# Kernel tuning notes

Hardware: AMD Instinct MI355X
Metric: run time of the kernel (lower is better)

Reference implementation:

```python
import jax, jax.numpy as jnp
import numpy as np

# Block sizes: 3-hop sampled bipartite graphs (src -> dst per layer)
N_SRC0, N_DST0, E0 = 500_000, 100_000, 1_000_000
N_DST1, E1 = 10_000, 100_000
N_DST2, E2 = 1_024, 10_240
D_IN, D_HID, N_CLS = 128, 128, 47


def setup_inputs() -> dict:
    key = jax.random.key(0)
    ks = jax.random.split(key, 16)
    feats = jax.random.normal(ks[0], (N_SRC0, D_IN), dtype=jnp.float32)
    src0 = jax.random.randint(ks[1], (E0,), 0, N_SRC0)
    dst0 = jax.random.randint(ks[2], (E0,), 0, N_DST0)
    src1 = jax.random.randint(ks[3], (E1,), 0, N_DST0)
    dst1 = jax.random.randint(ks[4], (E1,), 0, N_DST1)
    src2 = jax.random.randint(ks[5], (E2,), 0, N_DST1)
    dst2 = jax.random.randint(ks[6], (E2,), 0, N_DST2)
    # fsi.inverse_idx reindex + NPFeatureShuffle all-to-all -> two permutations
    inverse_idx = jax.random.permutation(ks[7], N_DST0)
    shuffle_idx = jax.random.permutation(ks[8], N_DST0)
    def glorot(k, fan_in, fan_out):
        lim = np.sqrt(6.0 / (fan_in + fan_out)).astype(np.float32)
        return jax.random.uniform(k, (fan_in, fan_out), jnp.float32, -lim, lim)
    W0 = glorot(ks[9], D_IN, D_HID)
    b0 = jnp.zeros((D_HID,), jnp.float32)
    W1 = glorot(ks[10], D_HID, D_HID)
    b1 = jnp.zeros((D_HID,), jnp.float32)
    W2 = glorot(ks[11], D_HID, N_CLS)
    b2 = jnp.zeros((N_CLS,), jnp.float32)
    return dict(feats=feats, src0=src0, dst0=dst0, src1=src1, dst1=dst1,
                src2=src2, dst2=dst2, inverse_idx=inverse_idx,
                shuffle_idx=shuffle_idx, W0=W0, b0=b0, W1=W1, b1=b1, W2=W2, b2=b2)


def _graph_conv(h_src, src, dst, n_src, n_dst, W, b, norm_both):
    # DGL GraphConv: optional D^{-1/2} on src, W, sum-aggregate over edges,
    # optional D^{-1/2} on dst, + bias. Degrees clamped to min 1.
    ones = jnp.ones(src.shape[0], dtype=h_src.dtype)
    if norm_both:
        out_deg = jax.ops.segment_sum(ones, src, num_segments=n_src)
        h_src = h_src * jax.lax.rsqrt(jnp.clip(out_deg, 1.0, None))[:, None]
    msgs = (h_src @ W)[src]                      # [E, d_out] gather
    agg = jax.ops.segment_sum(msgs, dst, num_segments=n_dst)  # scatter-add
    if norm_both:
        in_deg = jax.ops.segment_sum(ones, dst, num_segments=n_dst)
        agg = agg * jax.lax.rsqrt(jnp.clip(in_deg, 1.0, None))[:, None]
    return agg + b


def reference(feats, src0, dst0, src1, dst1, src2, dst2,
              inverse_idx, shuffle_idx, W0, b0, W1, b1, W2, b2):
    # layer 0: norm='none'
    h = _graph_conv(feats, src0, dst0, N_SRC0, N_DST0, W0, b0, norm_both=False)
    # fsi.inverse_idx reindex + NPFeatureShuffle (modeled as permutations)
    h = h[inverse_idx]
    h = h[shuffle_idx]
    h = jax.nn.relu(h)  # dropout is identity in eval
    # layer 1: norm='both'
    h = _graph_conv(h, src1, dst1, N_DST0, N_DST1, W1, b1, norm_both=True)
    h = jax.nn.relu(h)
    # layer 2: norm='both'
    h = _graph_conv(h, src2, dst2, N_DST1, N_DST2, W2, b2, norm_both=True)
    return h
```

## Files before the change

### kernel.cpp

```cpp
#include <hip/hip_runtime.h>
#include <stdint.h>

typedef unsigned int u32;
typedef unsigned short u16;
typedef __attribute__((ext_vector_type(8))) short short8;
typedef __attribute__((ext_vector_type(4))) float f32x4;

#define N_SRC0 500000
#define N_DST0 100000
#define N_DST1 10000
#define N_DST2 1024
#define NCLS 47

#define NB0 98
#define NB1 10
#define NB2 1
#define NBLK 109

static __device__ __forceinline__ float bf16_lo(u32 v) { return __uint_as_float(v << 16); }
static __device__ __forceinline__ float bf16_hi(u32 v) { return __uint_as_float(v & 0xffff0000u); }
static __device__ __forceinline__ float bf16_to_f(u16 s) { return __uint_as_float(((u32)s) << 16); }
static __device__ __forceinline__ u16 f_to_bf16(float f) {
    u32 u = __float_as_uint(f);
    u32 r = u + 0x7fffu + ((u >> 16) & 1u);
    return (u16)(r >> 16);
}

#define OFF_X1     0u
#define OFF_X2     51200000u
#define OFF_CSR0   56320000u
#define OFF_CSR1   60320000u
#define OFF_CSR2   60720000u
#define OFF_RS0    60760960u
#define OFF_CUR0   61160976u
#define OFF_RS1    61560976u
#define OFF_CUR1   61600992u
#define OFF_RS2    61640992u
#define OFF_CUR2   61645104u
#define OFF_CNT0   61649200u
#define OFF_DS1    62049200u
#define OFF_DD1    62449200u
#define OFF_DS2    62489200u
#define OFF_DD2    62529200u
#define ZERO_OFF   OFF_CNT0
#define ZERO_N4    55256u
#define OFF_WF0    62533296u
#define OFF_WF1    62598832u
#define OFF_WC2    62664368u
#define OFF_BC0    62688432u
#define OFF_BC1    62688944u
#define OFF_BC2    62689456u
#define OFF_FLAG   62689712u
#define OFF_BSUM   62689776u
#define OFF_BOFF   62690224u

__global__ __launch_bounds__(256) void k_prep(
    const u32* __restrict__ feats_w,
    const void* __restrict__ W0, const void* __restrict__ b0,
    const void* __restrict__ W1, const void* __restrict__ b1,
    const void* __restrict__ W2, const void* __restrict__ b2,
    float4* __restrict__ zbase,
    u16* __restrict__ wf0, u16* __restrict__ wf1,
    float* __restrict__ wc2, float* __restrict__ bc0,
    float* __restrict__ bc1, float* __restrict__ bc2,
    u32* __restrict__ flag)
{
    int b = blockIdx.x, t = threadIdx.x;
    if (b < 216) {
        u32 i = b * 256 + t;
        if (i < ZERO_N4) zbase[i] = make_float4(0.f, 0.f, 0.f, 0.f);
        return;
    }
    if (b == 216) {
        if (t < 64) {
            u32 u = feats_w[t];
            int e = (u >> 23) & 0xff;
            unsigned long long m = __ballot(e >= 0xC0);
            if (t == 0) *flag = (m != 0ull) ? 1u : 0u;
        }
        return;
    }
    __shared__ u32 lflag;
    if (b < 233) {
        const void* W = (b < 225) ? W0 : W1;
        u16* dst = (b < 225) ? wf0 : wf1;
        int base = ((b < 225) ? (b - 217) : (b - 225)) * 256;
        if (t == 0) lflag = 0u;
        __syncthreads();
        if (t < 64) { u32 u = ((const u32*)W)[t]; if (((u >> 23) & 0xff) >= 0xC0) atomicOr(&lflag, 1u); }
        __syncthreads();
        bool bf = (lflag != 0u);
        int idx = base + t;
        int fid = idx >> 6, lane = idx & 63;
        int nt = fid >> 2, ks = fid & 3;
        #pragma unroll
        for (int j = 0; j < 8; ++j) {
            int k = ks * 32 + (lane >> 4) * 8 + j;
            int n = nt * 16 + (lane & 15);
            u16 v = bf ? ((const u16*)W)[k * 128 + n]
                       : f_to_bf16(((const float*)W)[k * 128 + n]);
            dst[idx * 8 + j] = v;
        }
        return;
    }
    if (b < 257) {
        if (t == 0) lflag = 0u;
        __syncthreads();
        if (t < 64) { u32 u = ((const u32*)W2)[t]; if (((u >> 23) & 0xff) >= 0xC0) atomicOr(&lflag, 1u); }
        __syncthreads();
        bool bf = (lflag != 0u);
        int i = (b - 233) * 256 + t;
        if (i < 128 * NCLS)
            wc2[i] = bf ? bf16_to_f(((const u16*)W2)[i]) : ((const float*)W2)[i];
        return;
    }
    if (t < 128) { bc0[t] = ((const float*)b0)[t]; bc1[t] = ((const float*)b1)[t]; }
    if (t < NCLS) bc2[t] = ((const float*)b2)[t];
}

__global__ __launch_bounds__(256) void k_deg_all(
    const int* __restrict__ dst0,
    const int* __restrict__ src1, const int* __restrict__ dst1,
    const int* __restrict__ src2, const int* __restrict__ dst2,
    u32* __restrict__ cnt0, u32* __restrict__ dS1, u32* __restrict__ dD1,
    u32* __restrict__ dS2, u32* __restrict__ dD2, int E0, int E1, int E2)
{
    int i = blockIdx.x * 256 + threadIdx.x;
    if (i < E0) atomicAdd(&cnt0[dst0[i]], 1u);
    if (i < E1) { atomicAdd(&dS1[src1[i]], 1u); atomicAdd(&dD1[dst1[i]], 1u); }
    if (i < E2) { atomicAdd(&dS2[src2[i]], 1u); atomicAdd(&dD2[dst2[i]], 1u); }
}

static __device__ __forceinline__ void seg_map(int b, const u32* cnt0, const u32* dD1,
                                               const u32* dD2, const u32*& cnt,
                                               int& base, int& n, int& seg) {
    if (b < NB0)            { cnt = cnt0; base = b * 1024;          n = N_DST0; seg = 0; }
    else if (b < NB0 + NB1) { cnt = dD1;  base = (b - NB0) * 1024;  n = N_DST1; seg = 1; }
    else                    { cnt = dD2;  base = 0;                 n = N_DST2; seg = 2; }
}

__global__ __launch_bounds__(256) void k_bsum(
    const u32* __restrict__ cnt0, const u32* __restrict__ dD1,
    const u32* __restrict__ dD2, u32* __restrict__ bsum)
{
    const u32* cnt; int base, n, seg;
    seg_map(blockIdx.x, cnt0, dD1, dD2, cnt, base, n, seg);
    int t = threadIdx.x;
    int i0 = base + t * 4;
    u32 s = 0;
    #pragma unroll
    for (int j = 0; j < 4; ++j) { int i = i0 + j; if (i < n) s += cnt[i]; }
    #pragma unroll
    for (int off = 32; off; off >>= 1) s += __shfl_down(s, off, 64);
    __shared__ u32 wsum[4];
    if ((t & 63) == 0) wsum[t >> 6] = s;
    __syncthreads();
    if (t == 0) bsum[blockIdx.x] = wsum[0] + wsum[1] + wsum[2] + wsum[3];
}

__global__ void k_bscan(const u32* __restrict__ bsum, u32* __restrict__ boff,
                        u32* __restrict__ rs0, u32* __restrict__ rs1,
                        u32* __restrict__ rs2)
{
    if (threadIdx.x != 0) return;
    u32 run = 0;
    for (int b = 0; b < NB0; ++b) { boff[b] = run; run += bsum[b]; }
    rs0[N_DST0] = run;
    run = 0;
    for (int b = NB0; b < NB0 + NB1; ++b) { boff[b] = run; run += bsum[b]; }
    rs1[N_DST1] = run;
    boff[NB0 + NB1] = 0;
    rs2[N_DST2] = bsum[NB0 + NB1];
}

__global__ __launch_bounds__(256) void k_bwrite(
    const u32* __restrict__ cnt0, const u32* __restrict__ dD1,
    const u32* __restrict__ dD2, const u32* __restrict__ boff,
    u32* __restrict__ rs0, u32* __restrict__ cur0,
    u32* __restrict__ rs1, u32* __restrict__ cur1,
    u32* __restrict__ rs2, u32* __restrict__ cur2)
{
    const u32* cnt; int base, n, seg;
    seg_map(blockIdx.x, cnt0, dD1, dD2, cnt, base, n, seg);
    u32 *rs, *cur;
    if (seg == 0)      { rs = rs0; cur = cur0; }
    else if (seg == 1) { rs = rs1; cur = cur1; }
    else               { rs = rs2; cur = cur2; }

    int t = threadIdx.x;
    int i0 = base + t * 4;
    u32 c[4]; u32 s = 0;
    #pragma unroll
    for (int j = 0; j < 4; ++j) {
        int i = i0 + j;
        c[j] = (i < n) ? cnt[i] : 0u;
        s += c[j];
    }
    __shared__ u32 sc[256];
    sc[t] = s;
    __syncthreads();
    #pragma unroll
    for (int off = 1; off < 256; off <<= 1) {
        u32 v = (t >= off) ? sc[t - off] : 0u;
        __syncthreads();
        sc[t] += v;
        __syncthreads();
    }
    u32 ex = sc[t] - s + boff[blockIdx.x];
    #pragma unroll
    for (int j = 0; j < 4; ++j) {
        int i = i0 + j;
        if (i < n) { rs[i] = ex; cur[i] = ex; ex += c[j]; }
    }
}

__global__ __launch_bounds__(256) void k_fill(
    const int* __restrict__ src0, const int* __restrict__ dst0,
    const int* __restrict__ src1, const int* __restrict__ dst1,
    const int* __restrict__ src2, const int* __restrict__ dst2,
    u32* __restrict__ cur0, int* __restrict__ csr0,
    u32* __restrict__ cur1, int* __restrict__ csr1,
    u32* __restrict__ cur2, int* __restrict__ csr2,
    int E0, int E1, int E2)
{
    int i = blockIdx.x * 256 + threadIdx.x;
    if (i < E0) { u32 p = atomicAdd(&cur0[dst0[i]], 1u); csr0[p] = src0[i]; }
    if (i < E1) { u32 p = atomicAdd(&cur1[dst1[i]], 1u); csr1[p] = src1[i]; }
    if (i < E2) { u32 p = atomicAdd(&cur2[dst2[i]], 1u); csr2[p] = src2[i]; }
}

__global__ __launch_bounds__(256) void k_layer(
    const void* __restrict__ Ain, const u32* __restrict__ flag,
    const u32* __restrict__ rs, const int* __restrict__ csr,
    const int* __restrict__ inv, const int* __restrict__ shuf,
    const u32* __restrict__ preDeg, const u32* __restrict__ postDeg,
    const u16* __restrict__ Wfrag, const float* __restrict__ bias,
    float* __restrict__ out, int rows)
{
    __shared__ u16  As[48][136];
    __shared__ int  rowmapS[48];
    __shared__ float preS[48], postS[48], bS[128];

    int tid = threadIdx.x;
    int wv = tid >> 6, lane = tid & 63;
    int I0 = blockIdx.x * 48;

    if (tid < 48) {
        int I = I0 + tid;
        int ar = 0; float pre = 1.f, post = 1.f;
        if (I < rows) {
            ar = shuf ? inv[shuf[I]] : I;
            if (preDeg)  { u32 d = preDeg[I];  pre  = rsqrtf((float)(d > 1u ? d : 1u)); }
            if (postDeg) { u32 d = postDeg[I]; post = rsqrtf((float)(d > 1u ? d : 1u)); }
        }
        rowmapS[tid] = ar; preS[tid] = pre; postS[tid] = post;
    }
    if (tid < 128) bS[tid] = bias[tid];

    short8 bf[2][4];
    #pragma unroll
    for (int nt = 0; nt < 2; ++nt)
        #pragma unroll
        for (int ks = 0; ks < 4; ++ks) {
            int fid = (wv * 2 + nt) * 4 + ks;
            bf[nt][ks] = *(const short8*)(Wfrag + (size_t)(fid * 64 + lane) * 8);
        }
    __syncthreads();

    bool bfp = flag && (*flag != 0u);
    for (int i = 0; i < 12; ++i) {
        int r = wv * 12 + i;
        int I = I0 + r;
        float x = 0.f, y = 0.f;
        if (I < rows) {
            int ar = rowmapS[r];
            u32 e = rs[ar], end = rs[ar + 1];
            if (bfp) {
                const u32* f = (const u32*)Ain;
                for (; e + 4 <= end; e += 4) {
                    int s0 = csr[e], s1 = csr[e+1], s2 = csr[e+2], s3 = csr[e+3];
                    u32 v0 = f[(size_t)s0 * 64 + lane];
                    u32 v1 = f[(size_t)s1 * 64 + lane];
                    u32 v2 = f[(size_t)s2 * 64 + lane];
                    u32 v3 = f[(size_t)s3 * 64 + lane];
                    x += bf16_lo(v0) + bf16_lo(v1) + bf16_lo(v2) + bf16_lo(v3);
                    y += bf16_hi(v0) + bf16_hi(v1) + bf16_hi(v2) + bf16_hi(v3);
                }
                for (; e < end; ++e) {
                    u32 v = f[(size_t)csr[e] * 64 + lane];
                    x += bf16_lo(v); y += bf16_hi(v);
                }
            } else {
                const float2* f = (const float2*)Ain;
                for (; e + 4 <= end; e += 4) {
                    int s0 = csr[e], s1 = csr[e+1], s2 = csr[e+2], s3 = csr[e+3];
                    float2 v0 = f[(size_t)s0 * 64 + lane];
                    float2 v1 = f[(size_t)s1 * 64 + lane];
                    float2 v2 = f[(size_t)s2 * 64 + lane];
                    float2 v3 = f[(size_t)s3 * 64 + lane];
                    x += v0.x + v1.x + v2.x + v3.x;
                    y += v0.y + v1.y + v2.y + v3.y;
                }
                for (; e < end; ++e) {
                    float2 v = f[(size_t)csr[e] * 64 + lane];
                    x += v.x; y += v.y;
                }
            }
        }
        u32 pk = ((u32)f_to_bf16(y) << 16) | (u32)f_to_bf16(x);
        *(u32*)&As[r][2 * lane] = pk;
    }
    __syncthreads();

    f32x4 acc[2][3];
    #pragma unroll
    for (int nt = 0; nt < 2; ++nt)
        #pragma unroll
        for (int mt = 0; mt < 3; ++mt) acc[nt][mt] = (f32x4){0.f, 0.f, 0.f, 0.f};

    #pragma unroll
    for (int ks = 0; ks < 4; ++ks) {
        short8 af[3];
        #pragma unroll
        for (int mt = 0; mt < 3; ++mt) {
            int row = mt * 16 + (lane & 15);
            int k0 = ks * 32 + (lane >> 4) * 8;
            af[mt] = *(const short8*)&As[row][k0];
        }
        #pragma unroll
        for (int nt = 0; nt < 2; ++nt)
            #pragma unroll
            for (int mt = 0; mt < 3; ++mt)
                acc[nt][mt] = __builtin_amdgcn_mfma_f32_16x16x32_bf16(
                    af[mt], bf[nt][ks], acc[nt][mt], 0, 0, 0);
    }

    int quad = lane >> 4, cl = lane & 15;
    #pragma unroll
    for (int nt = 0; nt < 2; ++nt) {
        int col = (wv * 2 + nt) * 16 + cl;
        float bb = bS[col];
        #pragma unroll
        for (int mt = 0; mt < 3; ++mt) {
            #pragma unroll
            for (int rg = 0; rg < 4; ++rg) {
                int lr = mt * 16 + quad * 4 + rg;
                int I = I0 + lr;
                if (I < rows) {
                    float v = acc[nt][mt][rg] * preS[lr] + bb;
                    v = v > 0.f ? v : 0.f;
                    out[(size_t)I * 128 + col] = v * postS[lr];
                }
            }
        }
    }
}

__global__ __launch_bounds__(256) void k_layer2(
    const float2* __restrict__ x2, const u32* __restrict__ rs,
    const int* __restrict__ csr, const u32* __restrict__ preDeg,
    const float* __restrict__ Wc2, const float* __restrict__ bc2,
    void* __restrict__ out, const u32* __restrict__ flag)
{
    __shared__ float t2[16][128];
    int tid = threadIdx.x;
    int wv = tid >> 6, lane = tid & 63;
    int R0 = blockIdx.x * 16;

    for (int i = 0; i < 4; ++i) {
        int r = wv * 4 + i;
        int R = R0 + r;
        float x = 0.f, y = 0.f;
        u32 e = rs[R], end = rs[R + 1];
        for (; e + 4 <= end; e += 4) {
            int s0 = csr[e], s1 = csr[e+1], s2 = csr[e+2], s3 = csr[e+3];
            float2 v0 = x2[(size_t)s0 * 64 + lane];
            float2 v1 = x2[(size_t)s1 * 64 + lane];
            float2 v2 = x2[(size_t)s2 * 64 + lane];
            float2 v3 = x2[(size_t)s3 * 64 + lane];
            x += v0.x + v1.x + v2.x + v3.x;
            y += v0.y + v1.y + v2.y + v3.y;
        }
        for (; e < end; ++e) {
            float2 v = x2[(size_t)csr[e] * 64 + lane];
            x += v.x; y += v.y;
        }
        t2[r][2 * lane] = x;
        t2[r][2 * lane + 1] = y;
    }
    __syncthreads();

    bool bfp = flag && (*flag != 0u);
    for (int idx = tid; idx < 16 * NCLS; idx += 256) {
        int r = idx / NCLS, c = idx - NCLS * r;
        float a = 0.f;
        #pragma unroll 8
        for (int k = 0; k < 128; ++k) a = fmaf(t2[r][k], Wc2[k * NCLS + c], a);
        u32 d = preDeg[R0 + r];
        float v = a * rsqrtf((float)(d > 1u ? d : 1u)) + bc2[c];
        int g = (R0 + r) * NCLS + c;
        if (bfp) ((u16*)out)[g] = f_to_bf16(v);
        else     ((float*)out)[g] = v;
    }
}

extern "C" void kernel_launch(void* const* d_in, const int* in_sizes, int n_in,
                              void* d_out, int out_size, void* d_ws, size_t ws_size,
                              hipStream_t stream)
{
    (void)n_in; (void)out_size; (void)ws_size;
    const void* feats = d_in[0];
    const int* src0 = (const int*)d_in[1];
    const int* dst0 = (const int*)d_in[2];
    const int* src1 = (const int*)d_in[3];
    const int* dst1 = (const int*)d_in[4];
    const int* src2 = (const int*)d_in[5];
    const int* dst2 = (const int*)d_in[6];
    const int* inv  = (const int*)d_in[7];
    const int* shuf = (const int*)d_in[8];
    const void* W0 = d_in[9];  const void* b0 = d_in[10];
    const void* W1 = d_in[11]; const void* b1 = d_in[12];
    const void* W2 = d_in[13]; const void* b2 = d_in[14];
    int E0 = in_sizes[1], E1 = in_sizes[3], E2 = in_sizes[5];

    char* ws = (char*)d_ws;
    float* x1  = (float*)(ws + OFF_X1);
    float* x2  = (float*)(ws + OFF_X2);
    int* csr0 = (int*)(ws + OFF_CSR0);
    int* csr1 = (int*)(ws + OFF_CSR1);
    int* csr2 = (int*)(ws + OFF_CSR2);
    u32* rs0  = (u32*)(ws + OFF_RS0);
    u32* cur0 = (u32*)(ws + OFF_CUR0);
    u32* rs1  = (u32*)(ws + OFF_RS1);
    u32* cur1 = (u32*)(ws + OFF_CUR1);
    u32* rs2  = (u32*)(ws + OFF_RS2);
    u32* cur2 = (u32*)(ws + OFF_CUR2);
    u32* cnt0 = (u32*)(ws + OFF_CNT0);
    u32* dS1  = (u32*)(ws + OFF_DS1);
    u32* dD1  = (u32*)(ws + OFF_DD1);
    u32* dS2  = (u32*)(ws + OFF_DS2);
    u32* dD2  = (u32*)(ws + OFF_DD2);
    u16* wf0  = (u16*)(ws + OFF_WF0);
    u16* wf1  = (u16*)(ws + OFF_WF1);
    float* wc2 = (float*)(ws + OFF_WC2);
    float* bc0 = (float*)(ws + OFF_BC0);
    float* bc1 = (float*)(ws + OFF_BC1);
    float* bc2 = (float*)(ws + OFF_BC2);
    u32* flag  = (u32*)(ws + OFF_FLAG);
    u32* bsum  = (u32*)(ws + OFF_BSUM);
    u32* boff  = (u32*)(ws + OFF_BOFF);

    k_prep<<<258, 256, 0, stream>>>((const u32*)feats, W0, b0, W1, b1, W2, b2,
                                    (float4*)(ws + ZERO_OFF), wf0, wf1, wc2,
                                    bc0, bc1, bc2, flag);
    k_deg_all<<<(E0 + 255) / 256, 256, 0, stream>>>(dst0, src1, dst1, src2, dst2,
                                                    cnt0, dS1, dD1, dS2, dD2, E0, E1, E2);
    k_bsum<<<NBLK, 256, 0, stream>>>(cnt0, dD1, dD2, bsum);
    k_bscan<<<1, 64, 0, stream>>>(bsum, boff, rs0, rs1, rs2);
    k_bwrite<<<NBLK, 256, 0, stream>>>(cnt0, dD1, dD2, boff,
                                       rs0, cur0, rs1, cur1, rs2, cur2);
    k_fill<<<(E0 + 255) / 256, 256, 0, stream>>>(src0, dst0, src1, dst1, src2, dst2,
                                                 cur0, csr0, cur1, csr1, cur2, csr2,
                                                 E0, E1, E2);
    k_layer<<<(N_DST0 + 47) / 48, 256, 0, stream>>>(
        feats, flag, rs0, csr0, inv, shuf, nullptr, dS1, wf0, bc0, x1, N_DST0);
    k_layer<<<(N_DST1 + 47) / 48, 256, 0, stream>>>(
        x1, nullptr, rs1, csr1, nullptr, nullptr, dD1, dS2, wf1, bc1, x2, N_DST1);
    k_layer2<<<N_DST2 / 16, 256, 0, stream>>>(
        (const float2*)x2, rs2, csr2, dD2, wc2, bc2, d_out, flag);
}
```

Measured before the change: 681.9 us.

## Flatten per-wave edge lists into a shared queue for batched gathers

Each wave now stages the neighbor indices of its 12 rows into a shared edge queue tagged with row id. It then gathers eight edges at a time across row boundaries and accumulates into an fp32 shared tile with LDS atomics, with an overflow loop for rows beyond the staging cap. The goal is to raise memory-level parallelism for low-degree rows, where per-row loops leave few loads in flight. The cost is LDS atomics, more shared memory (a fp32 tile plus the queue), which may cut occupancy, and an in-place bf16 repack of the tile.

Measured after the change: 1.272 ms. 1.87x slower.

```diff
diff --git a/kernel.cpp b/kernel.cpp
--- a/kernel.cpp
+++ b/kernel.cpp
@@ -14,8 +14,9 @@
 
 #define NB0 98
 #define NB1 10
-#define NB2 1
 #define NBLK 109
+
+#define EQCAP 384
 
 static __device__ __forceinline__ float bf16_lo(u32 v) { return __uint_as_float(v << 16); }
 static __device__ __forceinline__ float bf16_hi(u32 v) { return __uint_as_float(v & 0xffff0000u); }
@@ -237,78 +238,111 @@
     const u16* __restrict__ Wfrag, const float* __restrict__ bias,
     float* __restrict__ out, int rows)
 {
-    __shared__ u16  As[48][136];
-    __shared__ int  rowmapS[48];
+    __shared__ __align__(16) float Af[48][136];
+    __shared__ u32  eqS[4 * EQCAP];
+    __shared__ u32  rowBegS[48], rowCntS[48], stgS[48];
     __shared__ float preS[48], postS[48], bS[128];
 
     int tid = threadIdx.x;
     int wv = tid >> 6, lane = tid & 63;
     int I0 = blockIdx.x * 48;
+    int r0 = wv * 12;
 
     if (tid < 48) {
         int I = I0 + tid;
-        int ar = 0; float pre = 1.f, post = 1.f;
+        u32 beg = 0, cnt = 0; float pre = 1.f, post = 1.f;
         if (I < rows) {
-            ar = shuf ? inv[shuf[I]] : I;
+            int ar = shuf ? inv[shuf[I]] : I;
+            beg = rs[ar]; cnt = rs[ar + 1] - beg;
             if (preDeg)  { u32 d = preDeg[I];  pre  = rsqrtf((float)(d > 1u ? d : 1u)); }
             if (postDeg) { u32 d = postDeg[I]; post = rsqrtf((float)(d > 1u ? d : 1u)); }
         }
-        rowmapS[tid] = ar; preS[tid] = pre; postS[tid] = post;
+        rowBegS[tid] = beg; rowCntS[tid] = cnt;
+        preS[tid] = pre; postS[tid] = post;
     }
     if (tid < 128) bS[tid] = bias[tid];
-
-    short8 bf[2][4];
+    for (int i = tid; i < 48 * 136; i += 256) ((float*)Af)[i] = 0.f;
+
+    short8 bfr[2][4];
     #pragma unroll
     for (int nt = 0; nt < 2; ++nt)
         #pragma unroll
         for (int ks = 0; ks < 4; ++ks) {
             int fid = (wv * 2 + nt) * 4 + ks;
-            bf[nt][ks] = *(const short8*)(Wfrag + (size_t)(fid * 64 + lane) * 8);
+            bfr[nt][ks] = *(const short8*)(Wfrag + (size_t)(fid * 64 + lane) * 8);
         }
     __syncthreads();
 
+    u32* eqw = eqS + wv * EQCAP;
+    int off = 0;
+    for (int i = 0; i < 12; ++i) {
+        int r = r0 + i;
+        int cnt = (int)rowCntS[r];
+        int take = cnt > 64 ? 64 : cnt;
+        if (off + take > EQCAP) take = (EQCAP > off) ? (EQCAP - off) : 0;
+        if (lane == 0) stgS[r] = (u32)take;
+        if (lane < take) {
+            int s = csr[rowBegS[r] + lane];
+            eqw[off + lane] = ((u32)i << 26) | (u32)s;
+        }
+        off += take;
+    }
+    int W = off;
+
     bool bfp = flag && (*flag != 0u);
+    for (int base = 0; base < W; base += 8) {
+        u32 pk[8];
+        #pragma unroll
+        for (int j = 0; j < 8; ++j) {
+            int ii = base + j; if (ii >= W) ii = W - 1;
+            pk[j] = eqw[ii];
+        }
+        float xx[8], yy[8];
+        if (bfp) {
+            const u32* f = (const u32*)Ain;
+            #pragma unroll
+            for (int j = 0; j < 8; ++j) {
+                u32 v = f[(size_t)(pk[j] & 0x03ffffffu) * 64 + lane];
+                xx[j] = bf16_lo(v); yy[j] = bf16_hi(v);
+            }
+        } else {
+            const float2* f = (const float2*)Ain;
+            #pragma unroll
+            for (int j = 0; j < 8; ++j) {
+                float2 v = f[(size_t)(pk[j] & 0x03ffffffu) * 64 + lane];
+                xx[j] = v.x; yy[j] = v.y;
+            }
+        }
+        #pragma unroll
+        for (int j = 0; j < 8; ++j) {
+            if (base + j < W) {
+                int r = r0 + (int)(pk[j] >> 26);
+                atomicAdd(&Af[r][2 * lane],     xx[j]);
+                atomicAdd(&Af[r][2 * lane + 1], yy[j]);
+            }
+        }
+    }
+
     for (int i = 0; i < 12; ++i) {
-        int r = wv * 12 + i;
-        int I = I0 + r;
-        float x = 0.f, y = 0.f;
-        if (I < rows) {
-            int ar = rowmapS[r];
-            u32 e = rs[ar], end = rs[ar + 1];
-            if (bfp) {
-                const u32* f = (const u32*)Ain;
-                for (; e + 4 <= end; e += 4) {
-                    int s0 = csr[e], s1 = csr[e+1], s2 = csr[e+2], s3 = csr[e+3];
-                    u32 v0 = f[(size_t)s0 * 64 + lane];
-                    u32 v1 = f[(size_t)s1 * 64 + lane];
-                    u32 v2 = f[(size_t)s2 * 64 + lane];
-                    u32 v3 = f[(size_t)s3 * 64 + lane];
-                    x += bf16_lo(v0) + bf16_lo(v1) + bf16_lo(v2) + bf16_lo(v3);
-                    y += bf16_hi(v0) + bf16_hi(v1) + bf16_hi(v2) + bf16_hi(v3);
-                }
-                for (; e < end; ++e) {
-                    u32 v = f[(size_t)csr[e] * 64 + lane];
-                    x += bf16_lo(v); y += bf16_hi(v);
-                }
-            } else {
-                const float2* f = (const float2*)Ain;
-                for (; e + 4 <= end; e += 4) {
-                    int s0 = csr[e], s1 = csr[e+1], s2 = csr[e+2], s3 = csr[e+3];
-                    float2 v0 = f[(size_t)s0 * 64 + lane];
-                    float2 v1 = f[(size_t)s1 * 64 + lane];
-                    float2 v2 = f[(size_t)s2 * 64 + lane];
-                    float2 v3 = f[(size_t)s3 * 64 + lane];
-                    x += v0.x + v1.x + v2.x + v3.x;
-                    y += v0.y + v1.y + v2.y + v3.y;
-                }
-                for (; e < end; ++e) {
-                    float2 v = f[(size_t)csr[e] * 64 + lane];
-                    x += v.x; y += v.y;
-                }
-            }
-        }
-        u32 pk = ((u32)f_to_bf16(y) << 16) | (u32)f_to_bf16(x);
-        *(u32*)&As[r][2 * lane] = pk;
+        int r = r0 + i;
+        int cnt = (int)rowCntS[r], st = (int)stgS[r];
+        u32 beg = rowBegS[r];
+        for (int e = st; e < cnt; ++e) {
+            int s = csr[beg + e];
+            float x, y;
+            if (bfp) { u32 v = ((const u32*)Ain)[(size_t)s * 64 + lane]; x = bf16_lo(v); y = bf16_hi(v); }
+            else     { float2 v = ((const float2*)Ain)[(size_t)s * 64 + lane]; x = v.x; y = v.y; }
+            atomicAdd(&Af[r][2 * lane],     x);
+            atomicAdd(&Af[r][2 * lane + 1], y);
+        }
+    }
+
+    u16* Ab = (u16*)Af;
+    for (int i = 0; i < 12; ++i) {
+        int r = r0 + i;
+        float x = Af[r][2 * lane], y = Af[r][2 * lane + 1];
+        u32 pkd = ((u32)f_to_bf16(y) << 16) | (u32)f_to_bf16(x);
+        ((u32*)(Ab + (size_t)r * 272))[lane] = pkd;
     }
     __syncthreads();
 
@@ -325,14 +359,14 @@
         for (int mt = 0; mt < 3; ++mt) {
             int row = mt * 16 + (lane & 15);
             int k0 = ks * 32 + (lane >> 4) * 8;
-            af[mt] = *(const short8*)&As[row][k0];
+            af[mt] = *(const short8*)(Ab + (size_t)row * 272 + k0);
         }
         #pragma unroll
         for (int nt = 0; nt < 2; ++nt)
             #pragma unroll
             for (int mt = 0; mt < 3; ++mt)
                 acc[nt][mt] = __builtin_amdgcn_mfma_f32_16x16x32_bf16(
-                    af[mt], bf[nt][ks], acc[nt][mt], 0, 0, 0);
+                    af[mt], bfr[nt][ks], acc[nt][mt], 0, 0, 0);
     }
 
     int quad = lane >> 4, cl = lane & 15;
```
